# Kernel tuning notes

Measured on AMD Instinct MI355X. Metric: run time of the kernel, lower is better.

The kernel has to match this reference:

```python
import jax, jax.numpy as jnp
import numpy as np

N, E, D, R, L = 100000, 800000, 64, 7, 3
HID, KH = D // 4, 32          # IEConv hidden = dims[i]//4, kernel_hidden_dim = 32
EDGE_DIM = 14
BN_EPS = 1e-5
LN_EPS = 1e-5


def _normalize(v, eps=1e-12):
    n = jnp.linalg.norm(v, axis=-1, keepdims=True)
    return v / jnp.maximum(n, eps)


def _bn(h, p):
    # eval-mode BatchNorm1d; p: [4, dim] = (gamma, beta, running_mean, running_var)
    return (h - p[2]) * jax.lax.rsqrt(p[3] + BN_EPS) * p[0] + p[1]


def setup_inputs() -> dict:
    key = jax.random.key(0)
    keys = iter(jax.random.split(key, 40))
    nk = lambda: next(keys)
    par = lambda shape, s=0.1: jax.random.normal(nk(), shape, jnp.float32) * s

    def bn_par(dim):
        g = 1.0 + 0.1 * jax.random.normal(nk(), (L, dim), jnp.float32)
        b = 0.1 * jax.random.normal(nk(), (L, dim), jnp.float32)
        m = 0.1 * jax.random.normal(nk(), (L, dim), jnp.float32)
        v = 0.5 + jax.random.uniform(nk(), (L, dim), jnp.float32)
        return jnp.stack([g, b, m, v], axis=1)  # [L,4,dim]

    inp = {
        "x": jax.random.normal(nk(), (N, D), jnp.float32),
        "pos": jax.random.normal(nk(), (N, 3), jnp.float32) * 10.0,
        "edge_index": jax.random.randint(nk(), (2, E), 0, N),
        "edge_relation": jax.random.randint(nk(), (E,), 0, R),
        # GeometricRelationalGraphConv params (per layer)
        "W_rel": par((L, R * D, D)), "b_rel": par((L, D)),
        "W_self": par((L, D, D)), "b_self": par((L, D)),
        # IEConvLayer params
        "W_l1": par((L, D, HID)), "b_l1": par((L, HID)),
        "W_k1": par((L, EDGE_DIM, KH)), "b_k1": par((L, KH)),
        "W_k2": par((L, KH, (HID + 1) * HID)), "b_k2": par((L, (HID + 1) * HID)),
        "W_l2": par((L, HID, D)), "b_l2": par((L, D)),
        "bn_in": bn_par(D), "bn_msg": bn_par(HID), "bn_upd": bn_par(HID), "bn_out": bn_par(D),
        "ln_g": 1.0 + 0.1 * jax.random.normal(nk(), (L, D), jnp.float32),
        "ln_b": 0.1 * jax.random.normal(nk(), (L, D), jnp.float32),
    }
    return inp


def _forward(x, pos, W_rel, b_rel, W_self, b_self, W_l1, b_l1, W_k1, b_k1,
             W_k2, b_k2, W_l2, b_l2, bn_in, bn_msg, bn_upd, bn_out, ln_g, ln_b,
             edge_index, edge_relation):
    node_in, node_out = edge_index[0], edge_index[1]
    # ---- get_ieconv_edge_feature ----
    ones3 = jnp.ones((1, 3), x.dtype)
    u = _normalize(jnp.concatenate([ones3, pos[1:] - pos[:-1]], axis=0))        # [N,3]
    b = _normalize(jnp.concatenate([u[:-1] - u[1:], ones3], axis=0))
    n = _normalize(jnp.concatenate([jnp.cross(u[:-1], u[1:]), ones3], axis=0))
    frame = jnp.stack([b, n, jnp.cross(b, n)], axis=-1)                          # [N,3,3]
    t = jnp.einsum('ejk,ej->ek', frame[node_in], pos[node_out] - pos[node_in])  # [E,3]
    r = jnp.sum(frame[node_in] * frame[node_out], axis=1)                        # [E,3]
    delta = (jnp.abs(node_in - node_out).astype(x.dtype) / 6.0)[:, None]         # atom2residue = arange
    edge_feat = jnp.concatenate(
        [t, r, delta, 1 - 2 * jnp.abs(t), 1 - 2 * jnp.abs(r), 1 - 2 * jnp.abs(delta)], axis=-1)  # [E,14]

    deg = jnp.maximum(
        jax.ops.segment_sum(jnp.ones_like(node_out, dtype=x.dtype), node_out, num_segments=N), 1.0)[:, None]
    seg = node_out * R + edge_relation
    h = x
    for i in range(L):
        # GeometricRelationalGraphConv: relation-bucketed scatter-sum, per-relation linear + self loop, relu
        upd = jax.ops.segment_sum(h[node_in], seg, num_segments=N * R).reshape(N, R * h.shape[-1])
        rel_out = jax.nn.relu(upd @ W_rel[i] + b_rel[i] + h @ W_self[i] + b_self[i])
        # IEConvLayer (eval mode, dropouts identity)
        li = jax.nn.relu(_bn(h, bn_in[i]))
        m = jax.nn.relu(_bn(li[node_in] @ W_l1[i] + b_l1[i], bn_msg[i]))         # [E,HID]
        ker = (jax.nn.relu(edge_feat @ W_k1[i] + b_k1[i]) @ W_k2[i] + b_k2[i]).reshape(-1, HID + 1, HID)
        m = jnp.einsum('ejk,ej->ek', ker[:, 1:, :], m) + ker[:, 0, :]            # per-edge kernel conv
        upd2 = jax.ops.segment_sum(m, node_out, num_segments=N) / deg            # scatter-mean
        upd2 = jax.nn.relu(_bn(upd2, bn_upd[i]))
        ie_out = _bn(upd2 @ W_l2[i] + b_l2[i], bn_out[i])
        hidden = rel_out + ie_out + h  # short_cut: shapes match at every layer
        mu = jnp.mean(hidden, axis=-1, keepdims=True)
        var = jnp.var(hidden, axis=-1, keepdims=True)
        h = (hidden - mu) * jax.lax.rsqrt(var + LN_EPS) * ln_g[i] + ln_b[i]
    return h


def reference(x, pos, edge_index, edge_relation, W_rel, b_rel, W_self, b_self,
              W_l1, b_l1, W_k1, b_k1, W_k2, b_k2, W_l2, b_l2,
              bn_in, bn_msg, bn_upd, bn_out, ln_g, ln_b):
    return _forward(x, pos, W_rel, b_rel, W_self, b_self, W_l1, b_l1, W_k1, b_k1,
                    W_k2, b_k2, W_l2, b_l2, bn_in, bn_msg, bn_upd, bn_out, ln_g, ln_b,
                    edge_index, edge_relation)
```

## Files before the change

kernel.cpp:

```cpp
#include <hip/hip_runtime.h>
#include <hip/hip_bf16.h>

typedef unsigned short u16;
typedef unsigned int   u32;

static const int Nn  = 100000;
static const int Ne  = 800000;
static const int Ll  = 3;
static const int SCAN_B = 98;

typedef short     short8  __attribute__((ext_vector_type(8)));
typedef float     floatx4 __attribute__((ext_vector_type(4)));

static const int H_CUM[19] = {
  0, 86016, 86208, 98496, 98688, 101760, 101808, 103152, 103248,
  129360, 130176, 133248, 133440, 134208, 134400, 134592, 135360, 135552, 135744
};
static const int H_SZ[18] = {
  86016, 192, 12288, 192, 3072, 48, 1344, 96,
  26112, 816, 3072, 192, 768, 192, 192, 768, 192, 192
};

union FU { u32 u; float f; };
__device__ __forceinline__ float b2f(u16 v) { FU x; x.u = ((u32)v) << 16; return x.f; }
__device__ __forceinline__ float lo2f(u32 w) { FU x; x.u = w << 16; return x.f; }
__device__ __forceinline__ float hi2f(u32 w) { FU x; x.u = w & 0xffff0000u; return x.f; }
__device__ __forceinline__ u16 f2b(float f) {
  FU x; x.f = f;
  u32 u = x.u;
  u32 r = (u + 0x7FFFu + ((u >> 16) & 1u)) >> 16;
  return (u16)r;
}
__device__ __forceinline__ u32 pk2(float a, float b) {
  __hip_bfloat162 h2 = __float22bfloat162_rn(make_float2(a, b));
  union { __hip_bfloat162 h; u32 u; } c; c.h = h2; return c.u;
}

__global__ void k_bnprep(const float* __restrict__ W, float* __restrict__ bnAB) {
  int idx = blockIdx.x * blockDim.x + threadIdx.x;
  if (idx >= 480) return;
  int i = idx / 160, d0 = idx % 160;
  const float* src; float* dstA; float* dstB; int dim, d;
  if (d0 < 64)       { d = d0;      src = W + 133440 + i * 256; dim = 64; dstA = bnAB + i*320 + 0;   dstB = bnAB + i*320 + 64;  }
  else if (d0 < 80)  { d = d0 - 64; src = W + 134208 + i * 64;  dim = 16; dstA = bnAB + i*320 + 128; dstB = bnAB + i*320 + 144; }
  else if (d0 < 96)  { d = d0 - 80; src = W + 134400 + i * 64;  dim = 16; dstA = bnAB + i*320 + 160; dstB = bnAB + i*320 + 176; }
  else               { d = d0 - 96; src = W + 134592 + i * 256; dim = 64; dstA = bnAB + i*320 + 192; dstB = bnAB + i*320 + 256; }
  float g = src[0*dim+d], b = src[1*dim+d], m = src[2*dim+d], v = src[3*dim+d];
  float A = g * rsqrtf(v + 1e-5f);
  float B = b - m * A;
  dstA[d] = A; dstB[d] = B;
}

__global__ void k_prep(const float* __restrict__ W, u16* __restrict__ BswG) {
  int i = blockIdx.x * 256 + threadIdx.x;
  if (i >= 3 * 8704) return;
  int layer = i / 8704, r = i % 8704;
  int jp = r / 512, l2 = r % 512;
  int lane = l2 / 8, j = l2 % 8;
  int q = (lane >> 4) * 8 + j, n = lane & 15;
  const float* Wk2 = W + 103248 + layer * 8704;
  BswG[i] = f2b(Wk2[q * 272 + jp * 16 + n]);
}

__global__ void k_prep2(const float* __restrict__ W, u16* __restrict__ B2) {
  int idx = blockIdx.x * 256 + threadIdx.x;
  if (idx >= 3 * 65536) return;
  int layer = idx >> 16, r = idx & 65535;
  int fr = r >> 9;
  int lane = (r >> 3) & 63, j = r & 7;
  int hl = fr & 1, ks = (fr >> 1) & 1, nt = (fr >> 2) & 3, nc = fr >> 4;
  int k = ks * 32 + (lane >> 4) * 8 + j;
  int g = nc * 64 + nt * 16 + (lane & 15);
  const float* Wrel  = W + layer * 28672;
  const float* Wself = W + 86208 + layer * 4096;
  float v = (g < 448) ? Wrel[((g >> 6) * 64 + k) * 64 + (g & 63)]
                      : Wself[k * 64 + (g - 448)];
  u16 hi = f2b(v);
  B2[idx] = hl ? f2b(v - b2f(hi)) : hi;
}

__global__ void k_prep3(const float* __restrict__ W, u16* __restrict__ Wk1f) {
  int idx = blockIdx.x * 256 + threadIdx.x;
  if (idx >= 3 * 2048) return;
  int layer = idx / 2048, r = idx % 2048;
  int kind = (r >> 10) & 1, nt = (r >> 9) & 1;
  int lane = (r >> 3) & 63, j = r & 7;
  int k = (lane >> 4) * 8 + j;
  int q = nt * 16 + (lane & 15);
  const float* Wk1 = W + 101808 + layer * 448;
  u16 out = 0;
  if (kind == 0) {
    if (k < 14)       out = f2b(Wk1[k * 32 + q]);
    else if (k < 28)  out = f2b(Wk1[(k - 14) * 32 + q]);
  } else {
    if (k < 14) {
      float w = Wk1[k * 32 + q];
      u16 hi = f2b(w);
      out = f2b(w - b2f(hi));
    }
  }
  Wk1f[idx] = out;
}

__global__ void k_u(const float* __restrict__ posf, float* __restrict__ u) {
  int i = blockIdx.x * blockDim.x + threadIdx.x;
  if (i >= Nn) return;
  float ux, uy, uz;
  if (i == 0) { ux = uy = uz = 0.57735026918962584f; }
  else {
    float vx = posf[i*3+0] - posf[(i-1)*3+0];
    float vy = posf[i*3+1] - posf[(i-1)*3+1];
    float vz = posf[i*3+2] - posf[(i-1)*3+2];
    float nrm = sqrtf(vx*vx + vy*vy + vz*vz);
    float inv = 1.0f / fmaxf(nrm, 1e-12f);
    ux = vx*inv; uy = vy*inv; uz = vz*inv;
  }
  u[i*3+0] = ux; u[i*3+1] = uy; u[i*3+2] = uz;
}

__global__ void k_frame(const float* __restrict__ u, float* __restrict__ frame) {
  int i = blockIdx.x * blockDim.x + threadIdx.x;
  if (i >= Nn) return;
  float bx, by, bz, nx, ny, nz;
  if (i < Nn - 1) {
    float ax = u[i*3+0], ay = u[i*3+1], az = u[i*3+2];
    float cx = u[(i+1)*3+0], cy = u[(i+1)*3+1], cz = u[(i+1)*3+2];
    float dx = ax-cx, dy = ay-cy, dz = az-cz;
    float n1 = sqrtf(dx*dx + dy*dy + dz*dz);
    float i1 = 1.0f / fmaxf(n1, 1e-12f);
    bx = dx*i1; by = dy*i1; bz = dz*i1;
    float qx = ay*cz - az*cy, qy = az*cx - ax*cz, qz = ax*cy - ay*cx;
    float n2 = sqrtf(qx*qx + qy*qy + qz*qz);
    float i2 = 1.0f / fmaxf(n2, 1e-12f);
    nx = qx*i2; ny = qy*i2; nz = qz*i2;
  } else {
    bx = by = bz = 0.57735026918962584f;
    nx = ny = nz = 0.57735026918962584f;
  }
  float ex = by*nz - bz*ny, ey = bz*nx - bx*nz, ez = bx*ny - by*nx;
  frame[i*9+0] = bx; frame[i*9+1] = nx; frame[i*9+2] = ex;
  frame[i*9+3] = by; frame[i*9+4] = ny; frame[i*9+5] = ey;
  frame[i*9+6] = bz; frame[i*9+7] = nz; frame[i*9+8] = ez;
}

__global__ void k_edge(const int* __restrict__ EI, const float* __restrict__ posf,
                       const float* __restrict__ frame,
                       float* __restrict__ t0, float* __restrict__ t1, float* __restrict__ t2,
                       float* __restrict__ r0, float* __restrict__ r1, float* __restrict__ r2,
                       int* __restrict__ cnt) {
  int e = blockIdx.x * 256 + threadIdx.x;
  int vin = EI[e], vout = EI[Ne + e];
  float fi[9], fo[9];
#pragma unroll
  for (int t = 0; t < 9; t++) fi[t] = frame[(size_t)vin*9 + t];
#pragma unroll
  for (int t = 0; t < 9; t++) fo[t] = frame[(size_t)vout*9 + t];
  float d0 = posf[vout*3+0] - posf[vin*3+0];
  float d1 = posf[vout*3+1] - posf[vin*3+1];
  float d2 = posf[vout*3+2] - posf[vin*3+2];
  float tt[3], rr[3];
#pragma unroll
  for (int k = 0; k < 3; k++) {
    tt[k] = fi[0*3+k]*d0 + fi[1*3+k]*d1 + fi[2*3+k]*d2;
    rr[k] = fi[0*3+k]*fo[0*3+k] + fi[1*3+k]*fo[1*3+k] + fi[2*3+k]*fo[2*3+k];
  }
  t0[e] = tt[0]; t1[e] = tt[1]; t2[e] = tt[2];
  r0[e] = rr[0]; r1[e] = rr[1]; r2[e] = rr[2];
  atomicAdd(&cnt[vout], 1);
}

__global__ __launch_bounds__(1024) void k_scan1(const int* __restrict__ cnt,
                                                int* __restrict__ locExc,
                                                int* __restrict__ btot) {
  __shared__ int sm[1024];
  int t = threadIdx.x, b = blockIdx.x;
  int i = b * 1024 + t;
  int v = (i < Nn) ? cnt[i] : 0;
  sm[t] = v;
  __syncthreads();
#pragma unroll
  for (int off = 1; off < 1024; off <<= 1) {
    int x = (t >= off) ? sm[t - off] : 0;
    __syncthreads();
    sm[t] += x;
    __syncthreads();
  }
  if (i < Nn) locExc[i] = sm[t] - v;
  if (t == 1023) btot[b] = sm[1023];
}

__global__ void k_scan2(const int* __restrict__ btot, int* __restrict__ boff,
                        int* __restrict__ rowptr) {
  if (threadIdx.x != 0 || blockIdx.x != 0) return;
  int run = 0;
  for (int b = 0; b < SCAN_B; b++) { boff[b] = run; run += btot[b]; }
  rowptr[Nn] = run;
}

__global__ void k_scan3(const int* __restrict__ cnt, const int* __restrict__ locExc,
                        const int* __restrict__ boff, int* __restrict__ rowptr,
                        float* __restrict__ deginv) {
  int i = blockIdx.x * blockDim.x + threadIdx.x;
  if (i >= Nn) return;
  rowptr[i] = locExc[i] + boff[i >> 10];
  int dv = cnt[i] > 1 ? cnt[i] : 1;
  deginv[i] = 1.0f / (float)dv;
}

__global__ void k_place(const int* __restrict__ EI, const int* __restrict__ EREL,
                        const int* __restrict__ rowptr,
                        int* __restrict__ fill, int* __restrict__ yidx,
                        int* __restrict__ inv) {
  int e = blockIdx.x * blockDim.x + threadIdx.x;
  if (e >= Ne) return;
  int vout = EI[Ne + e];
  int p = atomicAdd(&fill[vout], 1);
  int slot = rowptr[vout] + p;
  inv[e] = slot;
  yidx[slot] = EI[e] * 448 + EREL[e] * 64;
}

__global__ __launch_bounds__(256) void k_rel2(
    const float* __restrict__ h, const u16* __restrict__ Bsw,
    const float* __restrict__ brel, const float* __restrict__ bself,
    u16* __restrict__ Y, u16* __restrict__ S) {
  __shared__ uint4 bs4[1024];
  int tid = threadIdx.x;
  int w = tid >> 6, lane = tid & 63;
  int kq = lane >> 4, cl = lane & 15;
  int nb0 = blockIdx.x * 64;
  int anode = nb0 + w * 16 + cl;
  union U { uint4 u; short8 v; };

  uint4 Ah[2], Al[2];
#pragma unroll
  for (int ks = 0; ks < 2; ks++) {
    float p[8] = {0.f,0.f,0.f,0.f,0.f,0.f,0.f,0.f};
    if (anode < Nn) {
      const float4* hp = (const float4*)(h + (size_t)anode * 64 + ks * 32 + kq * 8);
      float4 q0 = hp[0], q1 = hp[1];
      p[0]=q0.x; p[1]=q0.y; p[2]=q0.z; p[3]=q0.w;
      p[4]=q1.x; p[5]=q1.y; p[6]=q1.z; p[7]=q1.w;
    }
    u32 hw[4], lw[4];
#pragma unroll
    for (int t = 0; t < 4; t++) {
      u16 ha = f2b(p[2*t]), hb = f2b(p[2*t+1]);
      hw[t] = (u32)ha | ((u32)hb << 16);
      lw[t] = pk2(p[2*t] - b2f(ha), p[2*t+1] - b2f(hb));
    }
    Ah[ks] = make_uint4(hw[0], hw[1], hw[2], hw[3]);
    Al[ks] = make_uint4(lw[0], lw[1], lw[2], lw[3]);
  }

  for (int nc = 0; nc < 8; nc++) {
    if (nc) __syncthreads();
    const uint4* src = (const uint4*)(Bsw + nc * 8192);
#pragma unroll
    for (int i = 0; i < 4; i++) bs4[tid + i * 256] = src[tid + i * 256];
    __syncthreads();

    floatx4 acc[4];
#pragma unroll
    for (int nt = 0; nt < 4; nt++) acc[nt] = (floatx4){0.f, 0.f, 0.f, 0.f};
#pragma unroll
    for (int nt = 0; nt < 4; nt++) {
#pragma unroll
      for (int ks = 0; ks < 2; ks++) {
        U bh, bl, ah, al;
        bh.u = bs4[((nt*2 + ks)*2 + 0)*64 + lane];
        bl.u = bs4[((nt*2 + ks)*2 + 1)*64 + lane];
        ah.u = Ah[ks]; al.u = Al[ks];
        acc[nt] = __builtin_amdgcn_mfma_f32_16x16x32_bf16(ah.v, bh.v, acc[nt], 0, 0, 0);
        acc[nt] = __builtin_amdgcn_mfma_f32_16x16x32_bf16(al.v, bh.v, acc[nt], 0, 0, 0);
        acc[nt] = __builtin_amdgcn_mfma_f32_16x16x32_bf16(ah.v, bl.v, acc[nt], 0, 0, 0);
      }
    }
    if (nc < 7) {
#pragma unroll
      for (int nt = 0; nt < 4; nt++) {
#pragma unroll
        for (int reg = 0; reg < 4; reg++) {
          int node = nb0 + w * 16 + kq * 4 + reg;
          if (node < Nn)
            Y[(size_t)node * 448 + nc * 64 + nt * 16 + cl] = f2b(acc[nt][reg]);
        }
      }
    } else {
#pragma unroll
      for (int nt = 0; nt < 4; nt++) {
        int c = nt * 16 + cl;
        float bias = brel[c] + bself[c];
#pragma unroll
        for (int reg = 0; reg < 4; reg++) {
          int node = nb0 + w * 16 + kq * 4 + reg;
          if (node < Nn)
            S[(size_t)node * 64 + c] = f2b(acc[nt][reg] + bias);
        }
      }
    }
  }
}

__global__ __launch_bounds__(256) void k_z(
    const float* __restrict__ h, const float* __restrict__ Wl1, const float* __restrict__ bl1,
    const float* __restrict__ bk2, const float* __restrict__ bn,
    u16* __restrict__ zt, u16* __restrict__ biast) {
  __shared__ float ls[64][65];
  __shared__ float zz[64][17];
  int tid = threadIdx.x;
  int nb0 = blockIdx.x * 64;
  const float* Ain = bn + 0;
  const float* Bin = bn + 64;
#pragma unroll
  for (int r = 0; r < 16; r++) {
    int idx = r * 256 + tid;
    int row = idx >> 6, col = idx & 63;
    int node = nb0 + row;
    float v = (node < Nn) ? h[(size_t)node * 64 + col] : 0.0f;
    ls[row][col] = fmaxf(v * Ain[col] + Bin[col], 0.0f);
  }
  __syncthreads();
  int row = tid >> 2, jq = (tid & 3) * 4;
  int node = nb0 + row;
  const float* Amsg = bn + 128;
  const float* Bmsg = bn + 144;
  float m1[4];
#pragma unroll
  for (int t = 0; t < 4; t++) m1[t] = bl1[jq + t];
  for (int c = 0; c < 64; c++) {
    float lv = ls[row][c];
#pragma unroll
    for (int t = 0; t < 4; t++) m1[t] += lv * Wl1[c * 16 + jq + t];
  }
  float zv[4];
#pragma unroll
  for (int t = 0; t < 4; t++) {
    zv[t] = fmaxf(m1[t] * Amsg[jq + t] + Bmsg[jq + t], 0.0f);
    zz[row][jq + t] = zv[t];
  }
  if (node < Nn) {
    u32* zg = (u32*)zt + (size_t)node * 8 + (tid & 3) * 2;
    zg[0] = pk2(zv[0], zv[1]);
    zg[1] = pk2(zv[2], zv[3]);
  }
  __syncthreads();
  float bb[4];
#pragma unroll
  for (int t = 0; t < 4; t++) bb[t] = bk2[jq + t];
  for (int j = 0; j < 16; j++) {
    float zj = zz[row][j];
#pragma unroll
    for (int t = 0; t < 4; t++) bb[t] += zj * bk2[(j + 1) * 16 + jq + t];
  }
  if (node < Nn) {
    u32* bg = (u32*)biast + (size_t)node * 8 + (tid & 3) * 2;
    bg[0] = pk2(bb[0], bb[1]);
    bg[1] = pk2(bb[2], bb[3]);
  }
}

__global__ __launch_bounds__(256) void k_msg(
    const float* __restrict__ t0, const float* __restrict__ t1, const float* __restrict__ t2,
    const float* __restrict__ r0, const float* __restrict__ r1, const float* __restrict__ r2,
    const int* __restrict__ EI, const int* __restrict__ inv,
    const u16* __restrict__ zt, const u16* __restrict__ biast,
    const u16* __restrict__ Wk1f, const float* __restrict__ bk1,
    const u16* __restrict__ BswG, u16* __restrict__ mo) {
  __shared__ u16 abuf[256 * 40];
  __shared__ u32 bsw[4352];
  __shared__ int ivin[256];

  int tid = threadIdx.x;
  int e0 = blockIdx.x * 256;
  int e = e0 + tid;

  for (int i = tid; i < 4352; i += 256) bsw[i] = ((const u32*)BswG)[i];

  int vin = EI[e], vout = EI[Ne + e];
  ivin[tid] = vin;

  float ef[14];
  ef[0] = t0[e]; ef[1] = t1[e]; ef[2] = t2[e];
  ef[3] = r0[e]; ef[4] = r1[e]; ef[5] = r2[e];
  int ad = vin - vout; if (ad < 0) ad = -ad;
  ef[6] = ((float)ad) / 6.0f;
#pragma unroll
  for (int k = 0; k < 7; k++) ef[7+k] = 1.0f - 2.0f*fabsf(ef[k]);

  u16 row[32];
#pragma unroll
  for (int d = 0; d < 14; d++) {
    u16 hi = f2b(ef[d]);
    row[d] = hi;
    row[14 + d] = f2b(ef[d] - b2f(hi));
  }
#pragma unroll
  for (int d = 28; d < 32; d++) row[d] = 0;
  u32* ar = (u32*)(abuf + (size_t)tid * 40);
#pragma unroll
  for (int i = 0; i < 16; i++)
    ar[i] = (u32)row[2*i] | ((u32)row[2*i+1] << 16);
  __syncthreads();

  int lane = tid & 63, w4 = (tid >> 6) * 4;
  int m = lane & 15, quad = lane >> 4;
  union U { uint4 u; short8 v; };

  U b0[2], b1[2];
#pragma unroll
  for (int nt = 0; nt < 2; nt++) {
    b0[nt].u = *(const uint4*)(Wk1f + 0*1024 + nt*512 + lane*8);
    b1[nt].u = *(const uint4*)(Wk1f + 1*1024 + nt*512 + lane*8);
  }
  float bk1v[2] = { bk1[m], bk1[16 + m] };

#pragma unroll
  for (int t = 0; t < 4; t++) {
    int s0 = (w4 + t) * 16;
    const u16* rs0 = abuf + (size_t)(s0 + m) * 40;

    U efr; efr.u = *(const uint4*)(rs0 + quad * 8);
#pragma unroll
    for (int nt = 0; nt < 2; nt++) {
      floatx4 aa = {0.f, 0.f, 0.f, 0.f};
      aa = __builtin_amdgcn_mfma_f32_16x16x32_bf16(efr.v, b0[nt].v, aa, 0, 0, 0);
      aa = __builtin_amdgcn_mfma_f32_16x16x32_bf16(efr.v, b1[nt].v, aa, 0, 0, 0);
#pragma unroll
      for (int reg = 0; reg < 4; reg++) {
        int se = s0 + quad * 4 + reg;
        float av = fmaxf(aa[reg] + bk1v[nt], 0.0f);
        abuf[(size_t)se * 40 + nt * 16 + m] = f2b(av);
      }
    }
    U afr; afr.u = *(const uint4*)(rs0 + quad * 8);

    int se0 = s0 + quad * 4;
    uint4 z0[4], z1[4]; float bv[4]; int sl[4];
#pragma unroll
    for (int reg = 0; reg < 4; reg++) {
      int vi = ivin[se0 + reg];
      const uint4* zp = (const uint4*)(zt + (size_t)vi * 16);
      z0[reg] = zp[0]; z1[reg] = zp[1];
      bv[reg] = b2f(biast[(size_t)vi * 16 + m]);
      sl[reg] = inv[e0 + se0 + reg];
    }

    float acc[4];
    {
      U bfr; bfr.u = *(const uint4*)(bsw + (size_t)lane * 4);
      floatx4 zz4 = {0.f, 0.f, 0.f, 0.f};
      floatx4 k0 = __builtin_amdgcn_mfma_f32_16x16x32_bf16(afr.v, bfr.v, zz4, 0, 0, 0);
#pragma unroll
      for (int reg = 0; reg < 4; reg++) acc[reg] = k0[reg];
    }
#pragma unroll
    for (int jp = 1; jp <= 16; jp++) {
      U bfr; bfr.u = *(const uint4*)(bsw + (size_t)(jp * 64 + lane) * 4);
      floatx4 zz4 = {0.f, 0.f, 0.f, 0.f};
      floatx4 kj = __builtin_amdgcn_mfma_f32_16x16x32_bf16(afr.v, bfr.v, zz4, 0, 0, 0);
      const int zi = jp - 1;
#pragma unroll
      for (int reg = 0; reg < 4; reg++) {
        const u32* zw = (zi < 8) ? (const u32*)&z0[reg] : (const u32*)&z1[reg];
        u32 wv = zw[(zi & 7) >> 1];
        float zv = (zi & 1) ? hi2f(wv) : lo2f(wv);
        acc[reg] += zv * kj[reg];
      }
    }
#pragma unroll
    for (int reg = 0; reg < 4; reg++)
      mo[(size_t)sl[reg] * 16 + m] = f2b(acc[reg] + bv[reg]);
  }
}

__global__ __launch_bounds__(256) void k_node(
    const float* __restrict__ h, const u16* __restrict__ S, const u16* __restrict__ Y,
    const int* __restrict__ rowptr, const int* __restrict__ yidx,
    const u16* __restrict__ mo, const float* __restrict__ deginv,
    const float* __restrict__ Wl2, const float* __restrict__ bl2,
    const float* __restrict__ bn, const float* __restrict__ lng, const float* __restrict__ lnb,
    float* __restrict__ hout) {
  __shared__ float relsm[4][64];
  __shared__ float u2s[4][16];
  int tid = threadIdx.x;
  int lane = tid & 63, w = tid >> 6;
  int n = blockIdx.x * 4 + w;
  bool act = (n < Nn);

  if (act) {
    int beg = rowptr[n], end = rowptr[n+1];

    int g = lane >> 3, col8 = lane & 7;
    float a8[8] = {0.f,0.f,0.f,0.f,0.f,0.f,0.f,0.f};
    for (int c0 = beg; c0 < end; c0 += 8) {
      int j = c0 + g;
      if (j < end) {
        int yoj = yidx[j];
        uint4 d = *(const uint4*)(Y + (size_t)yoj + col8 * 8);
        a8[0] += lo2f(d.x); a8[1] += hi2f(d.x);
        a8[2] += lo2f(d.y); a8[3] += hi2f(d.y);
        a8[4] += lo2f(d.z); a8[5] += hi2f(d.z);
        a8[6] += lo2f(d.w); a8[7] += hi2f(d.w);
      }
    }
#pragma unroll
    for (int t = 0; t < 8; t++) {
      a8[t] += __shfl_xor(a8[t],  8, 64);
      a8[t] += __shfl_xor(a8[t], 16, 64);
      a8[t] += __shfl_xor(a8[t], 32, 64);
    }
    if (lane < 8) {
#pragma unroll
      for (int t = 0; t < 8; t++) relsm[w][col8 * 8 + t] = a8[t];
    }

    int r = lane >> 2, c4 = lane & 3;
    float p4[4] = {0.f, 0.f, 0.f, 0.f};
    for (int p0 = beg; p0 < end; p0 += 16) {
      int p = p0 + r;
      if (p < end) {
        uint2 d = *(const uint2*)(mo + (size_t)p * 16 + c4 * 4);
        p4[0] += lo2f(d.x); p4[1] += hi2f(d.x);
        p4[2] += lo2f(d.y); p4[3] += hi2f(d.y);
      }
    }
#pragma unroll
    for (int t = 0; t < 4; t++) {
      p4[t] += __shfl_xor(p4[t],  4, 64);
      p4[t] += __shfl_xor(p4[t],  8, 64);
      p4[t] += __shfl_xor(p4[t], 16, 64);
      p4[t] += __shfl_xor(p4[t], 32, 64);
    }
    const float* Aupd = bn + 160;
    const float* Bupd = bn + 176;
    if (lane < 4) {
      float di = deginv[n];
#pragma unroll
      for (int t = 0; t < 4; t++) {
        int col = c4 * 4 + t;
        float v = p4[t] * di;
        u2s[w][col] = fmaxf(v * Aupd[col] + Bupd[col], 0.0f);
      }
    }
  }
  __syncthreads();
  if (act) {
    float rel_out = fmaxf(b2f(S[(size_t)n*64 + lane]) + relsm[w][lane], 0.0f);
    float ie = bl2[lane];
#pragma unroll
    for (int j = 0; j < 16; j++) ie += u2s[w][j] * Wl2[j*64 + lane];
    const float* Aout = bn + 192;
    const float* Bout = bn + 256;
    ie = ie * Aout[lane] + Bout[lane];
    float hidden = rel_out + ie + h[(size_t)n*64 + lane];
    float s = hidden;
#pragma unroll
    for (int off = 32; off > 0; off >>= 1) s += __shfl_xor(s, off, 64);
    float mu = s * (1.0f/64.0f);
    float d = hidden - mu;
    float s2 = d * d;
#pragma unroll
    for (int off = 32; off > 0; off >>= 1) s2 += __shfl_xor(s2, off, 64);
    float var = s2 * (1.0f/64.0f);
    float o = d * rsqrtf(var + 1e-5f) * lng[lane] + lnb[lane];
    hout[(size_t)n*64 + lane] = o;
  }
}

extern "C" void kernel_launch(void* const* d_in, const int* in_sizes, int n_in,
                              void* d_out, int out_size, void* d_ws, size_t ws_size,
                              hipStream_t stream) {
  const float* x    = (const float*)d_in[0];
  const float* posf = (const float*)d_in[1];
  const int* EI     = (const int*)d_in[2];
  const int* EREL   = (const int*)d_in[3];
  float* outf       = (float*)d_out;

  char* p = (char*)d_ws;
  auto alloc = [&](size_t bytes) -> char* {
    char* r = p;
    p += (bytes + 255) & ~((size_t)255);
    return r;
  };
  float* W      = (float*)alloc((size_t)135744 * 4);
  float* bnAB   = (float*)alloc((size_t)960 * 4);
  u16*   BswG   = (u16*)  alloc((size_t)3 * 8704 * 2);
  u16*   Bsw2   = (u16*)  alloc((size_t)3 * 65536 * 2);
  u16*   Wk1f   = (u16*)  alloc((size_t)3 * 2048 * 2);
  float* u      = (float*)alloc((size_t)Nn * 3 * 4);
  float* frame  = (float*)alloc((size_t)Nn * 9 * 4);
  int*   cnt    = (int*)  alloc((size_t)Nn * 4);
  int*   fill   = (int*)  alloc((size_t)Nn * 4);
  int*   rowptr = (int*)  alloc((size_t)(Nn + 1) * 4);
  int*   locExc = (int*)  alloc((size_t)Nn * 4);
  int*   btot   = (int*)  alloc((size_t)SCAN_B * 4);
  int*   boff   = (int*)  alloc((size_t)SCAN_B * 4);
  int*   yidx   = (int*)  alloc((size_t)Ne * 4);
  int*   inv    = (int*)  alloc((size_t)Ne * 4);
  float* deginv = (float*)alloc((size_t)Nn * 4);
  float* h      = (float*)alloc((size_t)Nn * 64 * 4);
  u16*   S      = (u16*)  alloc((size_t)Nn * 64 * 2);
  u16*   Y      = (u16*)  alloc((size_t)Nn * 448 * 2);
  u16*   mo     = (u16*)  alloc((size_t)Ne * 16 * 2);
  u16*   zt     = (u16*)  alloc((size_t)Nn * 16 * 2);
  u16*   biast  = (u16*)  alloc((size_t)Nn * 16 * 2);
  float* et0    = (float*)alloc((size_t)Ne * 4);
  float* et1    = (float*)alloc((size_t)Ne * 4);
  float* et2    = (float*)alloc((size_t)Ne * 4);
  float* er0    = (float*)alloc((size_t)Ne * 4);
  float* er1    = (float*)alloc((size_t)Ne * 4);
  float* er2    = (float*)alloc((size_t)Ne * 4);
  (void)n_in; (void)in_sizes; (void)out_size;

  size_t needed = (size_t)(p - (char*)d_ws);
  if (needed > ws_size) return;

  hipMemsetAsync(cnt,  0, (size_t)Nn * 4, stream);
  hipMemsetAsync(fill, 0, (size_t)Nn * 4, stream);

  for (int k = 0; k < 18; k++)
    hipMemcpyAsync(W + H_CUM[k], d_in[4 + k], (size_t)H_SZ[k] * 4,
                   hipMemcpyDeviceToDevice, stream);
  hipMemcpyAsync(h, x, (size_t)Nn * 64 * 4, hipMemcpyDeviceToDevice, stream);

  k_bnprep<<<2, 256, 0, stream>>>(W, bnAB);
  k_prep<<<(3*8704 + 255)/256, 256, 0, stream>>>(W, BswG);
  k_prep2<<<(3*65536 + 255)/256, 256, 0, stream>>>(W, Bsw2);
  k_prep3<<<(3*2048 + 255)/256, 256, 0, stream>>>(W, Wk1f);
  k_u<<<(Nn + 255)/256, 256, 0, stream>>>(posf, u);
  k_frame<<<(Nn + 255)/256, 256, 0, stream>>>(u, frame);
  k_edge<<<Ne/256, 256, 0, stream>>>(EI, posf, frame, et0, et1, et2, er0, er1, er2, cnt);
  k_scan1<<<SCAN_B, 1024, 0, stream>>>(cnt, locExc, btot);
  k_scan2<<<1, 64, 0, stream>>>(btot, boff, rowptr);
  k_scan3<<<(Nn + 255)/256, 256, 0, stream>>>(cnt, locExc, boff, rowptr, deginv);
  k_place<<<Ne/256, 256, 0, stream>>>(EI, EREL, rowptr, fill, yidx, inv);

  for (int i = 0; i < Ll; i++) {
    const float* brel  = W + H_CUM[1]  + i * 64;
    const float* bself = W + H_CUM[3]  + i * 64;
    const float* Wl1   = W + H_CUM[4]  + i * 1024;
    const float* bl1   = W + H_CUM[5]  + i * 16;
    const float* bk1   = W + H_CUM[7]  + i * 32;
    const float* bk2   = W + H_CUM[9]  + i * 272;
    const float* Wl2   = W + H_CUM[10] + i * 1024;
    const float* bl2   = W + H_CUM[11] + i * 64;
    const float* lng   = W + H_CUM[16] + i * 64;
    const float* lnb   = W + H_CUM[17] + i * 64;
    const float* bnL   = bnAB + i * 320;
    const u16*   BswL  = BswG + i * 8704;

    k_rel2<<<(Nn + 63)/64, 256, 0, stream>>>(h, Bsw2 + i * 65536, brel, bself, Y, S);
    k_z<<<(Nn + 63)/64, 256, 0, stream>>>(h, Wl1, bl1, bk2, bnL, zt, biast);
    k_msg<<<Ne/256, 256, 0, stream>>>(et0, et1, et2, er0, er1, er2, EI, inv,
                                      zt, biast, Wk1f + i * 2048, bk1, BswL, mo);
    k_node<<<(Nn + 3)/4, 256, 0, stream>>>(h, S, Y, rowptr, yidx, mo, deginv,
                                           Wl2, bl2, bnL, lng, lnb,
                                           (i == Ll - 1) ? outf : h);
  }
}
```

Measured before the change: 818.7 us.

## Aggregate neighbor features per relation before relational GEMM instead of transforming all nodes first

Replaces the transform-then-gather relational conv (per-node 448-wide Y matrix written to memory, then gathered per edge) with gather-then-transform: each node accumulates bf16 neighbor features into 7 relation buckets plus its own features, then runs one 512x64 MFMA GEMM in split-bf16 precision. This removes the large Y write and the wide per-edge gathers, at the cost of a lower-parallelism gather loop where each node's edges are walked serially by 16 lanes, plus a new bf16 copy of h. Numerics shift slightly since neighbor features are rounded to bf16 before summation.

```diff
diff --git a/kernel.cpp b/kernel.cpp
--- a/kernel.cpp
+++ b/kernel.cpp
@@ -62,21 +62,20 @@
   BswG[i] = f2b(Wk2[q * 272 + jp * 16 + n]);
 }
 
-__global__ void k_prep2(const float* __restrict__ W, u16* __restrict__ B2) {
+__global__ void k_prep2(const float* __restrict__ W, u16* __restrict__ B3) {
   int idx = blockIdx.x * 256 + threadIdx.x;
   if (idx >= 3 * 65536) return;
   int layer = idx >> 16, r = idx & 65535;
   int fr = r >> 9;
   int lane = (r >> 3) & 63, j = r & 7;
-  int hl = fr & 1, ks = (fr >> 1) & 1, nt = (fr >> 2) & 3, nc = fr >> 4;
+  int nt = fr & 3, hl = (fr >> 2) & 1, ks = fr >> 3;
   int k = ks * 32 + (lane >> 4) * 8 + j;
-  int g = nc * 64 + nt * 16 + (lane & 15);
+  int g = nt * 16 + (lane & 15);
   const float* Wrel  = W + layer * 28672;
   const float* Wself = W + 86208 + layer * 4096;
-  float v = (g < 448) ? Wrel[((g >> 6) * 64 + k) * 64 + (g & 63)]
-                      : Wself[k * 64 + (g - 448)];
+  float v = (k < 448) ? Wrel[k * 64 + g] : Wself[(k - 448) * 64 + g];
   u16 hi = f2b(v);
-  B2[idx] = hl ? f2b(v - b2f(hi)) : hi;
+  B3[idx] = hl ? f2b(v - b2f(hi)) : hi;
 }
 
 __global__ void k_prep3(const float* __restrict__ W, u16* __restrict__ Wk1f) {
@@ -217,95 +216,13 @@
   int p = atomicAdd(&fill[vout], 1);
   int slot = rowptr[vout] + p;
   inv[e] = slot;
-  yidx[slot] = EI[e] * 448 + EREL[e] * 64;
-}
-
-__global__ __launch_bounds__(256) void k_rel2(
-    const float* __restrict__ h, const u16* __restrict__ Bsw,
-    const float* __restrict__ brel, const float* __restrict__ bself,
-    u16* __restrict__ Y, u16* __restrict__ S) {
-  __shared__ uint4 bs4[1024];
-  int tid = threadIdx.x;
-  int w = tid >> 6, lane = tid & 63;
-  int kq = lane >> 4, cl = lane & 15;
-  int nb0 = blockIdx.x * 64;
-  int anode = nb0 + w * 16 + cl;
-  union U { uint4 u; short8 v; };
-
-  uint4 Ah[2], Al[2];
-#pragma unroll
-  for (int ks = 0; ks < 2; ks++) {
-    float p[8] = {0.f,0.f,0.f,0.f,0.f,0.f,0.f,0.f};
-    if (anode < Nn) {
-      const float4* hp = (const float4*)(h + (size_t)anode * 64 + ks * 32 + kq * 8);
-      float4 q0 = hp[0], q1 = hp[1];
-      p[0]=q0.x; p[1]=q0.y; p[2]=q0.z; p[3]=q0.w;
-      p[4]=q1.x; p[5]=q1.y; p[6]=q1.z; p[7]=q1.w;
-    }
-    u32 hw[4], lw[4];
-#pragma unroll
-    for (int t = 0; t < 4; t++) {
-      u16 ha = f2b(p[2*t]), hb = f2b(p[2*t+1]);
-      hw[t] = (u32)ha | ((u32)hb << 16);
-      lw[t] = pk2(p[2*t] - b2f(ha), p[2*t+1] - b2f(hb));
-    }
-    Ah[ks] = make_uint4(hw[0], hw[1], hw[2], hw[3]);
-    Al[ks] = make_uint4(lw[0], lw[1], lw[2], lw[3]);
-  }
-
-  for (int nc = 0; nc < 8; nc++) {
-    if (nc) __syncthreads();
-    const uint4* src = (const uint4*)(Bsw + nc * 8192);
-#pragma unroll
-    for (int i = 0; i < 4; i++) bs4[tid + i * 256] = src[tid + i * 256];
-    __syncthreads();
-
-    floatx4 acc[4];
-#pragma unroll
-    for (int nt = 0; nt < 4; nt++) acc[nt] = (floatx4){0.f, 0.f, 0.f, 0.f};
-#pragma unroll
-    for (int nt = 0; nt < 4; nt++) {
-#pragma unroll
-      for (int ks = 0; ks < 2; ks++) {
-        U bh, bl, ah, al;
-        bh.u = bs4[((nt*2 + ks)*2 + 0)*64 + lane];
-        bl.u = bs4[((nt*2 + ks)*2 + 1)*64 + lane];
-        ah.u = Ah[ks]; al.u = Al[ks];
-        acc[nt] = __builtin_amdgcn_mfma_f32_16x16x32_bf16(ah.v, bh.v, acc[nt], 0, 0, 0);
-        acc[nt] = __builtin_amdgcn_mfma_f32_16x16x32_bf16(al.v, bh.v, acc[nt], 0, 0, 0);
-        acc[nt] = __builtin_amdgcn_mfma_f32_16x16x32_bf16(ah.v, bl.v, acc[nt], 0, 0, 0);
-      }
-    }
-    if (nc < 7) {
-#pragma unroll
-      for (int nt = 0; nt < 4; nt++) {
-#pragma unroll
-        for (int reg = 0; reg < 4; reg++) {
-          int node = nb0 + w * 16 + kq * 4 + reg;
-          if (node < Nn)
-            Y[(size_t)node * 448 + nc * 64 + nt * 16 + cl] = f2b(acc[nt][reg]);
-        }
-      }
-    } else {
-#pragma unroll
-      for (int nt = 0; nt < 4; nt++) {
-        int c = nt * 16 + cl;
-        float bias = brel[c] + bself[c];
-#pragma unroll
-        for (int reg = 0; reg < 4; reg++) {
-          int node = nb0 + w * 16 + kq * 4 + reg;
-          if (node < Nn)
-            S[(size_t)node * 64 + c] = f2b(acc[nt][reg] + bias);
-        }
-      }
-    }
-  }
+  yidx[slot] = EI[e] * 8 + EREL[e];
 }
 
 __global__ __launch_bounds__(256) void k_z(
     const float* __restrict__ h, const float* __restrict__ Wl1, const float* __restrict__ bl1,
     const float* __restrict__ bk2, const float* __restrict__ bn,
-    u16* __restrict__ zt, u16* __restrict__ biast) {
+    u16* __restrict__ zt, u16* __restrict__ biast, u16* __restrict__ h16) {
   __shared__ float ls[64][65];
   __shared__ float zz[64][17];
   int tid = threadIdx.x;
@@ -318,6 +235,7 @@
     int row = idx >> 6, col = idx & 63;
     int node = nb0 + row;
     float v = (node < Nn) ? h[(size_t)node * 64 + col] : 0.0f;
+    if (node < Nn) h16[(size_t)node * 64 + col] = f2b(v);
     ls[row][col] = fmaxf(v * Ain[col] + Bin[col], 0.0f);
   }
   __syncthreads();
@@ -357,6 +275,93 @@
     u32* bg = (u32*)biast + (size_t)node * 8 + (tid & 3) * 2;
     bg[0] = pk2(bb[0], bb[1]);
     bg[1] = pk2(bb[2], bb[3]);
+  }
+}
+
+__global__ __launch_bounds__(256) void k_relagg(
+    const float* __restrict__ h, const u16* __restrict__ h16,
+    const int* __restrict__ rowptr, const int* __restrict__ yidx,
+    const u16* __restrict__ Bsw3,
+    const float* __restrict__ brel, const float* __restrict__ bself,
+    u16* __restrict__ rel16) {
+  __shared__ __align__(16) u16 uh[16][520];
+  __shared__ __align__(16) u16 ul[16][520];
+  int tid = threadIdx.x;
+  int w = tid >> 6, lane = tid & 63;
+  int grp = lane >> 4, cl = lane & 15;
+  int nb0 = blockIdx.x * 16;
+  int anode = nb0 + w * 4 + grp;
+  int lrow = w * 4 + grp;
+  union U { uint4 u; short8 v; };
+
+  float acc[7][4];
+#pragma unroll
+  for (int r = 0; r < 7; r++)
+#pragma unroll
+    for (int c = 0; c < 4; c++) acc[r][c] = 0.0f;
+  if (anode < Nn) {
+    int beg = rowptr[anode], end = rowptr[anode + 1];
+    for (int p = beg; p < end; p++) {
+      int ye = yidx[p];
+      int vin = ye >> 3, rl = ye & 7;
+      uint2 d = *(const uint2*)(h16 + (size_t)vin * 64 + cl * 4);
+      float v0 = lo2f(d.x), v1 = hi2f(d.x), v2 = lo2f(d.y), v3 = hi2f(d.y);
+#pragma unroll
+      for (int r = 0; r < 7; r++) {
+        bool hit = (rl == r);
+        acc[r][0] += hit ? v0 : 0.0f;
+        acc[r][1] += hit ? v1 : 0.0f;
+        acc[r][2] += hit ? v2 : 0.0f;
+        acc[r][3] += hit ? v3 : 0.0f;
+      }
+    }
+  }
+#pragma unroll
+  for (int r = 0; r < 7; r++) {
+#pragma unroll
+    for (int c = 0; c < 4; c++) {
+      float v = acc[r][c];
+      u16 hi = f2b(v);
+      uh[lrow][r * 64 + cl * 4 + c] = hi;
+      ul[lrow][r * 64 + cl * 4 + c] = f2b(v - b2f(hi));
+    }
+  }
+  {
+    float q[4] = {0.f, 0.f, 0.f, 0.f};
+    if (anode < Nn) {
+      float4 hv = ((const float4*)(h + (size_t)anode * 64))[cl];
+      q[0] = hv.x; q[1] = hv.y; q[2] = hv.z; q[3] = hv.w;
+    }
+#pragma unroll
+    for (int c = 0; c < 4; c++) {
+      u16 hi = f2b(q[c]);
+      uh[lrow][448 + cl * 4 + c] = hi;
+      ul[lrow][448 + cl * 4 + c] = f2b(q[c] - b2f(hi));
+    }
+  }
+  __syncthreads();
+
+  int quad = lane >> 4;
+  floatx4 o4 = {0.f, 0.f, 0.f, 0.f};
+  const u16* B0 = Bsw3 + (size_t)w * 512 + lane * 8;
+#pragma unroll
+  for (int ks = 0; ks < 16; ks++) {
+    U ah, al, bh, bl;
+    ah.u = *(const uint4*)(&uh[cl][ks * 32 + quad * 8]);
+    al.u = *(const uint4*)(&ul[cl][ks * 32 + quad * 8]);
+    bh.u = *(const uint4*)(B0 + (size_t)(ks * 2 + 0) * 2048);
+    bl.u = *(const uint4*)(B0 + (size_t)(ks * 2 + 1) * 2048);
+    o4 = __builtin_amdgcn_mfma_f32_16x16x32_bf16(ah.v, bh.v, o4, 0, 0, 0);
+    o4 = __builtin_amdgcn_mfma_f32_16x16x32_bf16(al.v, bh.v, o4, 0, 0, 0);
+    o4 = __builtin_amdgcn_mfma_f32_16x16x32_bf16(ah.v, bl.v, o4, 0, 0, 0);
+  }
+  int g = w * 16 + cl;
+  float bias = brel[g] + bself[g];
+#pragma unroll
+  for (int reg = 0; reg < 4; reg++) {
+    int node = nb0 + quad * 4 + reg;
+    if (node < Nn)
+      rel16[(size_t)node * 64 + g] = f2b(fmaxf(o4[reg] + bias, 0.0f));
   }
 }
 
@@ -475,13 +480,12 @@
 }
 
 __global__ __launch_bounds__(256) void k_node(
-    const float* __restrict__ h, const u16* __restrict__ S, const u16* __restrict__ Y,
-    const int* __restrict__ rowptr, const int* __restrict__ yidx,
+    const float* __restrict__ h, const u16* __restrict__ rel16,
+    const int* __restrict__ rowptr,
     const u16* __restrict__ mo, const float* __restrict__ deginv,
     const float* __restrict__ Wl2, const float* __restrict__ bl2,
     const float* __restrict__ bn, const float* __restrict__ lng, const float* __restrict__ lnb,
     float* __restrict__ hout) {
-  __shared__ float relsm[4][64];
   __shared__ float u2s[4][16];
   int tid = threadIdx.x;
   int lane = tid & 63, w = tid >> 6;
@@ -490,31 +494,6 @@
 
   if (act) {
     int beg = rowptr[n], end = rowptr[n+1];
-
-    int g = lane >> 3, col8 = lane & 7;
-    float a8[8] = {0.f,0.f,0.f,0.f,0.f,0.f,0.f,0.f};
-    for (int c0 = beg; c0 < end; c0 += 8) {
-      int j = c0 + g;
-      if (j < end) {
-        int yoj = yidx[j];
-        uint4 d = *(const uint4*)(Y + (size_t)yoj + col8 * 8);
-        a8[0] += lo2f(d.x); a8[1] += hi2f(d.x);
-        a8[2] += lo2f(d.y); a8[3] += hi2f(d.y);
-        a8[4] += lo2f(d.z); a8[5] += hi2f(d.z);
-        a8[6] += lo2f(d.w); a8[7] += hi2f(d.w);
-      }
-    }
-#pragma unroll
-    for (int t = 0; t < 8; t++) {
-      a8[t] += __shfl_xor(a8[t],  8, 64);
-      a8[t] += __shfl_xor(a8[t], 16, 64);
-      a8[t] += __shfl_xor(a8[t], 32, 64);
-    }
-    if (lane < 8) {
-#pragma unroll
-      for (int t = 0; t < 8; t++) relsm[w][col8 * 8 + t] = a8[t];
-    }
-
     int r = lane >> 2, c4 = lane & 3;
     float p4[4] = {0.f, 0.f, 0.f, 0.f};
     for (int p0 = beg; p0 < end; p0 += 16) {
@@ -546,7 +525,7 @@
   }
   __syncthreads();
   if (act) {
-    float rel_out = fmaxf(b2f(S[(size_t)n*64 + lane]) + relsm[w][lane], 0.0f);
+    float rel_out = b2f(rel16[(size_t)n*64 + lane]);
     float ie = bl2[lane];
 #pragma unroll
     for (int j = 0; j < 16; j++) ie += u2s[w][j] * Wl2[j*64 + lane];
@@ -586,7 +565,7 @@
   float* W      = (float*)alloc((size_t)135744 * 4);
   float* bnAB   = (float*)alloc((size_t)960 * 4);
   u16*   BswG   = (u16*)  alloc((size_t)3 * 8704 * 2);
-  u16*   Bsw2   = (u16*)  alloc((size_t)3 * 65536 * 2);
+  u16*   Bsw3   = (u16*)  alloc((size_t)3 * 65536 * 2);
   u16*   Wk1f   = (u16*)  alloc((size_t)3 * 2048 * 2);
   float* u      = (float*)alloc((size_t)Nn * 3 * 4);
   float* frame  = (float*)alloc((size_t)Nn * 9 * 4);
@@ -600,8 +579,8 @@
   int*   inv    = (int*)  alloc((size_t)Ne * 4);
   float* deginv = (float*)alloc((size_t)Nn * 4);
   float* h      = (float*)alloc((size_t)Nn * 64 * 4);
-  u16*   S      = (u16*)  alloc((size_t)Nn * 64 * 2);
-  u16*   Y      = (u16*)  alloc((size_t)Nn * 448 * 2);
+  u16*   h16    = (u16*)  alloc((size_t)Nn * 64 * 2);
+  u16*   rel16  = (u16*)  alloc((size_t)Nn * 64 * 2);
   u16*   mo     = (u16*)  alloc((size_t)Ne * 16 * 2);
   u16*   zt     = (u16*)  alloc((size_t)Nn * 16 * 2);
   u16*   biast  = (u16*)  alloc((size_t)Nn * 16 * 2);
@@ -626,7 +605,7 @@
 
   k_bnprep<<<2, 256, 0, stream>>>(W, bnAB);
   k_prep<<<(3*8704 + 255)/256, 256, 0, stream>>>(W, BswG);
-  k_prep2<<<(3*65536 + 255)/256, 256, 0, stream>>>(W, Bsw2);
+  k_prep2<<<(3*65536 + 255)/256, 256, 0, stream>>>(W, Bsw3);
   k_prep3<<<(3*2048 + 255)/256, 256, 0, stream>>>(W, Wk1f);
   k_u<<<(Nn + 255)/256, 256, 0, stream>>>(posf, u);
   k_frame<<<(Nn + 255)/256, 256, 0, stream>>>(u, frame);
@@ -650,11 +629,12 @@
     const float* bnL   = bnAB + i * 320;
     const u16*   BswL  = BswG + i * 8704;
 
-    k_rel2<<<(Nn + 63)/64, 256, 0, stream>>>(h, Bsw2 + i * 65536, brel, bself, Y, S);
-    k_z<<<(Nn + 63)/64, 256, 0, stream>>>(h, Wl1, bl1, bk2, bnL, zt, biast);
+    k_z<<<(Nn + 63)/64, 256, 0, stream>>>(h, Wl1, bl1, bk2, bnL, zt, biast, h16);
+    k_relagg<<<(Nn + 15)/16, 256, 0, stream>>>(h, h16, rowptr, yidx,
+                                               Bsw3 + i * 65536, brel, bself, rel16);
     k_msg<<<Ne/256, 256, 0, stream>>>(et0, et1, et2, er0, er1, er2, EI, inv,
                                       zt, biast, Wk1f + i * 2048, bk1, BswL, mo);
-    k_node<<<(Nn + 3)/4, 256, 0, stream>>>(h, S, Y, rowptr, yidx, mo, deginv,
+    k_node<<<(Nn + 3)/4, 256, 0, stream>>>(h, rel16, rowptr, mo, deginv,
                                            Wl2, bl2, bnL, lng, lnb,
                                            (i == Ll - 1) ? outf : h);
   }
```

After: 947.6 us. +15.8%, slower.
